# Optimization experiments

Measured on AMD Instinct MI355X. Metric: run time of the kernel, lower is better.

## Reference

```python
import jax, jax.numpy as jnp
import numpy as np

E_MAX = 8192  # fixed pad for the data-dependent edge count (jit-safe)
N_HITS = 8192


def setup_inputs() -> dict:
    key = jax.random.key(0)
    k1, k2, k3, k4, k5 = jax.random.split(key, 5)
    # columns: [event, x, y, z, station, track]
    r = jax.random.uniform(k1, (N_HITS,), minval=270.0, maxval=580.0)
    phi = jax.random.uniform(k2, (N_HITS,), minval=-3.1, maxval=3.1)
    # original uses phi = atan2(x, y), so x = r*sin(phi), y = r*cos(phi)
    x = r * jnp.sin(phi)
    y = r * jnp.cos(phi)
    z = jax.random.uniform(k3, (N_HITS,), minval=-2000.0, maxval=2000.0)
    station = jax.random.randint(k4, (N_HITS,), 0, 32).astype(jnp.float32)
    track = jax.random.randint(k5, (N_HITS,), 0, 1024).astype(jnp.float32)
    ev = jnp.zeros((N_HITS,), jnp.float32)  # single event -> one output graph
    event_data = jnp.stack([ev, x, y, z, station, track], axis=1)
    return {"event_data": event_data}


def _convert_normalize(event_data):
    # convert(): cartesian -> (r, phi, z); note atan2(x, y) as in the source
    x, y, z = event_data[:, 1], event_data[:, 2], event_data[:, 3]
    r = jnp.sqrt(x * x + y * y)
    phi = jnp.arctan2(x, y)
    # normalize() with hard-coded constraints [[269,581],[-3.15,3.15],[-2386,2386]]
    rn = 2.0 * (r - 269.0) / (581.0 - 269.0) - 1.0
    phin = 2.0 * (phi + 3.15) / (2.0 * 3.15) - 1.0
    zn = 2.0 * (z + 2386.0) / (2.0 * 2386.0) - 1.0
    return rn, phin, zn


def reference(event_data):
    rn, phin, zn = _convert_normalize(event_data)
    ev = event_data[:, 0].astype(jnp.int32)
    st = event_data[:, 4].astype(jnp.int32)
    # pair (i, j) valid iff same event and station_j == station_i + 1
    pair = (ev[:, None] == ev[None, :]) & (st[:, None] == (st[None, :] - 1))
    # merged[:, -2] = phi_j - phi_i ; merged[:, -1] = z_j - z_i (normalized coords)
    dphi = phin[None, :] - phin[:, None]  # [N, N]
    dz = zn[None, :] - zn[:, None]        # [N, N]
    valid = pair & (dphi > -0.04) & (dphi < 0.04) & (dz > -0.03) & (dz < 0.03)
    # torch.nonzero equivalent, padded to E_MAX (row-major order matches torch)
    src, dst = jnp.nonzero(valid, size=E_MAX, fill_value=0)
    count = jnp.sum(valid)
    edge_mask = jnp.arange(E_MAX) < count  # True for real edges, False for pads

    track = event_data[:, 5]
    # edges[:, [index_prev, index_current]] = track ids of (prev hit, next hit)
    edges = jnp.stack([track[src], track[dst]], axis=1)  # [E_MAX, 2]
    X = jnp.stack([rn, phin, zn], axis=1)  # hits[:, [1,2,3]] / 1.0
    # Ri/Ro: incidence via broadcast equality of track ids, as in the source
    Ri = ((track[:, None] == edges[None, :, 1]) & edge_mask[None, :]).astype(jnp.int32)
    Ro = ((track[:, None] == edges[None, :, 0]) & edge_mask[None, :]).astype(jnp.int32)
    y_lbl = jnp.zeros((E_MAX,), jnp.float32)
    return X, Ri, Ro, y_lbl, edges, edge_mask
```

## Files before the change

kernel.cpp:

```cpp
#include <hip/hip_runtime.h>

#define N_HITS 8192
#define E_MAX  8192
#define NSTA   32
#define NTRK   1024
#define NCHUNK 128

#define WS_HITA    0
#define WS_HTRACK  131072
#define WS_CAND    163840
#define WS_CCNT    294912
#define WS_COFF    311296
#define WS_BSTART  327680
#define WS_RCNT    327936
#define WS_ROFF    360704
#define WS_TCNT    393472
#define WS_TFILL   397568
#define WS_TOFF    401664
#define WS_THITS   405760

#define OFF_X  0
#define OFF_RI 24576
#define OFF_RO 67133440
#define OFF_Y  134242304
#define OFF_E  134250496
#define OFF_M  134266880

__global__ void k_pre(const float* __restrict__ ed, float* __restrict__ out,
                      float4* __restrict__ hitA, float* __restrict__ htrack,
                      int* __restrict__ ccnt, int* __restrict__ tcnt) {
    int h = blockIdx.x * blockDim.x + threadIdx.x;
    int lane = threadIdx.x & 63;
    int w = h >> 6;
    const float* row = ed + h * 6;
    float ev = row[0], x = row[1], y = row[2], z = row[3], stf = row[4], tr = row[5];
    float r   = sqrtf(x * x + y * y);
    float phi = atan2f(x, y);
    float rn   = 2.0f * (r   - 269.0f)  / 312.0f  - 1.0f;
    float phin = 2.0f * (phi + 3.15f)   / 6.3f    - 1.0f;
    float zn   = 2.0f * (z   + 2386.0f) / 4772.0f - 1.0f;
    out[OFF_X + h * 3 + 0] = rn;
    out[OFF_X + h * 3 + 1] = phin;
    out[OFF_X + h * 3 + 2] = zn;
    int st = (int)stf;
    hitA[h] = make_float4(phin, zn, (float)(int)ev, stf);
    htrack[h] = tr;
    for (int b = 0; b < NSTA; ++b) {
        unsigned long long m = __ballot(st == b);
        if (lane == 0) ccnt[b * NCHUNK + w] = __popcll(m);
    }
    atomicAdd(&tcnt[(int)tr], 1);
}

__global__ void k_scans(const int* __restrict__ ccnt, int* __restrict__ coff,
                        int* __restrict__ bstart,
                        const int* __restrict__ tcnt, int* __restrict__ toff) {
    __shared__ int sums[256];
    int tid = threadIdx.x;
    {
        int base = tid * 16;
        int loc[16]; int s = 0;
        for (int k = 0; k < 16; ++k) { loc[k] = ccnt[base + k]; s += loc[k]; }
        sums[tid] = s; __syncthreads();
        for (int d = 1; d < 256; d <<= 1) {
            int v = (tid >= d) ? sums[tid - d] : 0;
            __syncthreads();
            sums[tid] += v;
            __syncthreads();
        }
        int run = sums[tid] - s;
        for (int k = 0; k < 16; ++k) { coff[base + k] = run; run += loc[k]; }
        __syncthreads();
        if (tid < NSTA) bstart[tid] = coff[tid * NCHUNK];
        if (tid == 0)   bstart[NSTA] = N_HITS;
        __syncthreads();
    }
    {
        int base = tid * 4;
        int loc[4]; int s = 0;
        for (int k = 0; k < 4; ++k) { loc[k] = tcnt[base + k]; s += loc[k]; }
        sums[tid] = s; __syncthreads();
        for (int d = 1; d < 256; d <<= 1) {
            int v = (tid >= d) ? sums[tid - d] : 0;
            __syncthreads();
            sums[tid] += v;
            __syncthreads();
        }
        int run = sums[tid] - s;
        for (int k = 0; k < 4; ++k) { toff[base + k] = run; run += loc[k]; }
    }
}

__global__ void k_scatter(const float4* __restrict__ hitA, const float* __restrict__ htrack,
                          const int* __restrict__ coff, float4* __restrict__ cand,
                          const int* __restrict__ toff, int* __restrict__ tfill,
                          int* __restrict__ thits) {
    int h = blockIdx.x * blockDim.x + threadIdx.x;
    int lane = threadIdx.x & 63;
    int w = h >> 6;
    float4 a = hitA[h];
    float tr = htrack[h];
    int st = (int)a.w;
    for (int b = 0; b < NSTA; ++b) {
        unsigned long long m = __ballot(st == b);
        if (st == b) {
            int rank = __popcll(m & ((1ull << lane) - 1ull));
            cand[coff[b * NCHUNK + w] + rank] = make_float4(a.x, a.y, a.z, tr);
        }
    }
    int ti = (int)tr;
    int pos = atomicAdd(&tfill[ti], 1);
    thits[toff[ti] + pos] = h;
}

__device__ __forceinline__ bool edge_pred(float4 me, float4 cj) {
    float dphi = cj.x - me.x;
    float dz   = cj.y - me.y;
    return (cj.z == me.z) & (dphi > -0.04f) & (dphi < 0.04f)
                          & (dz > -0.03f) & (dz < 0.03f);
}

__global__ void k_rowcount(const float4* __restrict__ hitA, const float4* __restrict__ cand,
                           const int* __restrict__ bstart, int* __restrict__ rcnt) {
    int tid = threadIdx.x;
    int lane = tid & 63;
    int row = blockIdx.x * (blockDim.x >> 6) + (tid >> 6);
    float4 me = hitA[row];
    int b = (int)me.w + 1;
    int cnt = 0;
    if (b >= 1 && b < NSTA) {
        int s = bstart[b], e = bstart[b + 1];
        for (int k0 = s; k0 < e; k0 += 64) {
            int kk = k0 + lane;
            bool p = false;
            if (kk < e) p = edge_pred(me, cand[kk]);
            cnt += __popcll(__ballot(p));
        }
    }
    if (lane == 0) rcnt[row] = cnt;
}

__global__ void k_scanrows(const int* __restrict__ rcnt, int* __restrict__ roff,
                           const float* __restrict__ htrack, float* __restrict__ out) {
    __shared__ int sums[256];
    int tid = threadIdx.x;
    int base = tid * 32;
    int loc[32]; int s = 0;
    for (int k = 0; k < 32; ++k) { loc[k] = rcnt[base + k]; s += loc[k]; }
    sums[tid] = s; __syncthreads();
    for (int d = 1; d < 256; d <<= 1) {
        int v = (tid >= d) ? sums[tid - d] : 0;
        __syncthreads();
        sums[tid] += v;
        __syncthreads();
    }
    int run = sums[tid] - s;
    for (int k = 0; k < 32; ++k) { roff[base + k] = run; run += loc[k]; }
    __syncthreads();
    int S = sums[255];
    float t0 = htrack[0];
    for (int e = tid; e < E_MAX; e += 256) {
        bool v = e < S;
        out[OFF_M + e] = v ? 1.0f : 0.0f;
        if (!v) {
            out[OFF_E + 2 * e]     = t0;
            out[OFF_E + 2 * e + 1] = t0;
        }
    }
}

__global__ void k_emit(const float4* __restrict__ hitA, const float* __restrict__ htrack,
                       const float4* __restrict__ cand, const int* __restrict__ bstart,
                       const int* __restrict__ roff, const int* __restrict__ toff,
                       const int* __restrict__ tcnt, const int* __restrict__ thits,
                       float* __restrict__ out) {
    int tid = threadIdx.x;
    int lane = tid & 63;
    int row = blockIdx.x * (blockDim.x >> 6) + (tid >> 6);
    float4 me = hitA[row];
    int b = (int)me.w + 1;
    if (b < 1 || b >= NSTA) return;
    float tr_i = htrack[row];
    int bo = (int)tr_i;
    int os = toff[bo], oc = tcnt[bo];
    int s = bstart[b], e = bstart[b + 1];
    int base = roff[row];
    int c = 0;
    for (int k0 = s; k0 < e; k0 += 64) {
        int kk = k0 + lane;
        float4 cj = make_float4(0.f, 0.f, 0.f, 0.f);
        bool p = false;
        if (kk < e) { cj = cand[kk]; p = edge_pred(me, cj); }
        unsigned long long m = __ballot(p);
        if (p) {
            int idx = base + c + __popcll(m & ((1ull << lane) - 1ull));
            if (idx < E_MAX) {
                out[OFF_E + 2 * idx]     = tr_i;
                out[OFF_E + 2 * idx + 1] = cj.w;
                for (int j = 0; j < oc; ++j)
                    out[OFF_RO + (size_t)thits[os + j] * E_MAX + idx] = 1.0f;
                int bi = (int)cj.w;
                int is = toff[bi], ic = tcnt[bi];
                for (int j = 0; j < ic; ++j)
                    out[OFF_RI + (size_t)thits[is + j] * E_MAX + idx] = 1.0f;
            }
        }
        c += __popcll(m);
    }
}

extern "C" void kernel_launch(void* const* d_in, const int* in_sizes, int n_in,
                              void* d_out, int out_size, void* d_ws, size_t ws_size,
                              hipStream_t stream) {
    const float* ed = (const float*)d_in[0];
    float* out = (float*)d_out;
    char* ws = (char*)d_ws;

    float4* hitA   = (float4*)(ws + WS_HITA);
    float*  htrack = (float*) (ws + WS_HTRACK);
    float4* cand   = (float4*)(ws + WS_CAND);
    int*    ccnt   = (int*)   (ws + WS_CCNT);
    int*    coff   = (int*)   (ws + WS_COFF);
    int*    bstart = (int*)   (ws + WS_BSTART);
    int*    rcnt   = (int*)   (ws + WS_RCNT);
    int*    roffp  = (int*)   (ws + WS_ROFF);
    int*    tcnt   = (int*)   (ws + WS_TCNT);
    int*    tfill  = (int*)   (ws + WS_TFILL);
    int*    toff   = (int*)   (ws + WS_TOFF);
    int*    thits  = (int*)   (ws + WS_THITS);

    hipMemsetAsync(out + OFF_RI, 0, (size_t)(OFF_E - OFF_RI) * sizeof(float), stream);
    hipMemsetAsync(ws + WS_TCNT, 0, 2 * NTRK * sizeof(int), stream);

    hipLaunchKernelGGL(k_pre,      dim3(32),   dim3(256), 0, stream, ed, out, hitA, htrack, ccnt, tcnt);
    hipLaunchKernelGGL(k_scans,    dim3(1),    dim3(256), 0, stream, ccnt, coff, bstart, tcnt, toff);
    hipLaunchKernelGGL(k_scatter,  dim3(32),   dim3(256), 0, stream, hitA, htrack, coff, cand, toff, tfill, thits);
    hipLaunchKernelGGL(k_rowcount, dim3(2048), dim3(256), 0, stream, hitA, cand, bstart, rcnt);
    hipLaunchKernelGGL(k_scanrows, dim3(1),    dim3(256), 0, stream, rcnt, roffp, htrack, out);
    hipLaunchKernelGGL(k_emit,     dim3(2048), dim3(256), 0, stream, hitA, htrack, cand, bstart, roffp, toff, tcnt, thits, out);
}
```

Before: 556.4 us.

## Fuse six pipeline kernels into one cooperative kernel with grid syncs

Replaces the six separate launches (preprocess, scans, scatter, row count, row scan, emit) with a single cooperative kernel that separates phases using grid-wide syncs. The goal is to remove per-launch overhead and the gaps between dependent small kernels. In exchange, the grid shrinks to 256 blocks, so each wave handles 8 rows in the count and emit phases. This reduces parallelism for the latency-bound scattered writes, and single-block scan phases leave most of the grid idle at each barrier.

```diff
diff --git a/kernel.cpp b/kernel.cpp
--- a/kernel.cpp
+++ b/kernel.cpp
@@ -1,4 +1,6 @@
 #include <hip/hip_runtime.h>
+#include <hip/hip_cooperative_groups.h>
+namespace cg = cooperative_groups;
 
 #define N_HITS 8192
 #define E_MAX  8192
@@ -26,93 +28,6 @@
 #define OFF_E  134250496
 #define OFF_M  134266880
 
-__global__ void k_pre(const float* __restrict__ ed, float* __restrict__ out,
-                      float4* __restrict__ hitA, float* __restrict__ htrack,
-                      int* __restrict__ ccnt, int* __restrict__ tcnt) {
-    int h = blockIdx.x * blockDim.x + threadIdx.x;
-    int lane = threadIdx.x & 63;
-    int w = h >> 6;
-    const float* row = ed + h * 6;
-    float ev = row[0], x = row[1], y = row[2], z = row[3], stf = row[4], tr = row[5];
-    float r   = sqrtf(x * x + y * y);
-    float phi = atan2f(x, y);
-    float rn   = 2.0f * (r   - 269.0f)  / 312.0f  - 1.0f;
-    float phin = 2.0f * (phi + 3.15f)   / 6.3f    - 1.0f;
-    float zn   = 2.0f * (z   + 2386.0f) / 4772.0f - 1.0f;
-    out[OFF_X + h * 3 + 0] = rn;
-    out[OFF_X + h * 3 + 1] = phin;
-    out[OFF_X + h * 3 + 2] = zn;
-    int st = (int)stf;
-    hitA[h] = make_float4(phin, zn, (float)(int)ev, stf);
-    htrack[h] = tr;
-    for (int b = 0; b < NSTA; ++b) {
-        unsigned long long m = __ballot(st == b);
-        if (lane == 0) ccnt[b * NCHUNK + w] = __popcll(m);
-    }
-    atomicAdd(&tcnt[(int)tr], 1);
-}
-
-__global__ void k_scans(const int* __restrict__ ccnt, int* __restrict__ coff,
-                        int* __restrict__ bstart,
-                        const int* __restrict__ tcnt, int* __restrict__ toff) {
-    __shared__ int sums[256];
-    int tid = threadIdx.x;
-    {
-        int base = tid * 16;
-        int loc[16]; int s = 0;
-        for (int k = 0; k < 16; ++k) { loc[k] = ccnt[base + k]; s += loc[k]; }
-        sums[tid] = s; __syncthreads();
-        for (int d = 1; d < 256; d <<= 1) {
-            int v = (tid >= d) ? sums[tid - d] : 0;
-            __syncthreads();
-            sums[tid] += v;
-            __syncthreads();
-        }
-        int run = sums[tid] - s;
-        for (int k = 0; k < 16; ++k) { coff[base + k] = run; run += loc[k]; }
-        __syncthreads();
-        if (tid < NSTA) bstart[tid] = coff[tid * NCHUNK];
-        if (tid == 0)   bstart[NSTA] = N_HITS;
-        __syncthreads();
-    }
-    {
-        int base = tid * 4;
-        int loc[4]; int s = 0;
-        for (int k = 0; k < 4; ++k) { loc[k] = tcnt[base + k]; s += loc[k]; }
-        sums[tid] = s; __syncthreads();
-        for (int d = 1; d < 256; d <<= 1) {
-            int v = (tid >= d) ? sums[tid - d] : 0;
-            __syncthreads();
-            sums[tid] += v;
-            __syncthreads();
-        }
-        int run = sums[tid] - s;
-        for (int k = 0; k < 4; ++k) { toff[base + k] = run; run += loc[k]; }
-    }
-}
-
-__global__ void k_scatter(const float4* __restrict__ hitA, const float* __restrict__ htrack,
-                          const int* __restrict__ coff, float4* __restrict__ cand,
-                          const int* __restrict__ toff, int* __restrict__ tfill,
-                          int* __restrict__ thits) {
-    int h = blockIdx.x * blockDim.x + threadIdx.x;
-    int lane = threadIdx.x & 63;
-    int w = h >> 6;
-    float4 a = hitA[h];
-    float tr = htrack[h];
-    int st = (int)a.w;
-    for (int b = 0; b < NSTA; ++b) {
-        unsigned long long m = __ballot(st == b);
-        if (st == b) {
-            int rank = __popcll(m & ((1ull << lane) - 1ull));
-            cand[coff[b * NCHUNK + w] + rank] = make_float4(a.x, a.y, a.z, tr);
-        }
-    }
-    int ti = (int)tr;
-    int pos = atomicAdd(&tfill[ti], 1);
-    thits[toff[ti] + pos] = h;
-}
-
 __device__ __forceinline__ bool edge_pred(float4 me, float4 cj) {
     float dphi = cj.x - me.x;
     float dz   = cj.y - me.y;
@@ -120,102 +35,8 @@
                           & (dz > -0.03f) & (dz < 0.03f);
 }
 
-__global__ void k_rowcount(const float4* __restrict__ hitA, const float4* __restrict__ cand,
-                           const int* __restrict__ bstart, int* __restrict__ rcnt) {
-    int tid = threadIdx.x;
-    int lane = tid & 63;
-    int row = blockIdx.x * (blockDim.x >> 6) + (tid >> 6);
-    float4 me = hitA[row];
-    int b = (int)me.w + 1;
-    int cnt = 0;
-    if (b >= 1 && b < NSTA) {
-        int s = bstart[b], e = bstart[b + 1];
-        for (int k0 = s; k0 < e; k0 += 64) {
-            int kk = k0 + lane;
-            bool p = false;
-            if (kk < e) p = edge_pred(me, cand[kk]);
-            cnt += __popcll(__ballot(p));
-        }
-    }
-    if (lane == 0) rcnt[row] = cnt;
-}
-
-__global__ void k_scanrows(const int* __restrict__ rcnt, int* __restrict__ roff,
-                           const float* __restrict__ htrack, float* __restrict__ out) {
-    __shared__ int sums[256];
-    int tid = threadIdx.x;
-    int base = tid * 32;
-    int loc[32]; int s = 0;
-    for (int k = 0; k < 32; ++k) { loc[k] = rcnt[base + k]; s += loc[k]; }
-    sums[tid] = s; __syncthreads();
-    for (int d = 1; d < 256; d <<= 1) {
-        int v = (tid >= d) ? sums[tid - d] : 0;
-        __syncthreads();
-        sums[tid] += v;
-        __syncthreads();
-    }
-    int run = sums[tid] - s;
-    for (int k = 0; k < 32; ++k) { roff[base + k] = run; run += loc[k]; }
-    __syncthreads();
-    int S = sums[255];
-    float t0 = htrack[0];
-    for (int e = tid; e < E_MAX; e += 256) {
-        bool v = e < S;
-        out[OFF_M + e] = v ? 1.0f : 0.0f;
-        if (!v) {
-            out[OFF_E + 2 * e]     = t0;
-            out[OFF_E + 2 * e + 1] = t0;
-        }
-    }
-}
-
-__global__ void k_emit(const float4* __restrict__ hitA, const float* __restrict__ htrack,
-                       const float4* __restrict__ cand, const int* __restrict__ bstart,
-                       const int* __restrict__ roff, const int* __restrict__ toff,
-                       const int* __restrict__ tcnt, const int* __restrict__ thits,
-                       float* __restrict__ out) {
-    int tid = threadIdx.x;
-    int lane = tid & 63;
-    int row = blockIdx.x * (blockDim.x >> 6) + (tid >> 6);
-    float4 me = hitA[row];
-    int b = (int)me.w + 1;
-    if (b < 1 || b >= NSTA) return;
-    float tr_i = htrack[row];
-    int bo = (int)tr_i;
-    int os = toff[bo], oc = tcnt[bo];
-    int s = bstart[b], e = bstart[b + 1];
-    int base = roff[row];
-    int c = 0;
-    for (int k0 = s; k0 < e; k0 += 64) {
-        int kk = k0 + lane;
-        float4 cj = make_float4(0.f, 0.f, 0.f, 0.f);
-        bool p = false;
-        if (kk < e) { cj = cand[kk]; p = edge_pred(me, cj); }
-        unsigned long long m = __ballot(p);
-        if (p) {
-            int idx = base + c + __popcll(m & ((1ull << lane) - 1ull));
-            if (idx < E_MAX) {
-                out[OFF_E + 2 * idx]     = tr_i;
-                out[OFF_E + 2 * idx + 1] = cj.w;
-                for (int j = 0; j < oc; ++j)
-                    out[OFF_RO + (size_t)thits[os + j] * E_MAX + idx] = 1.0f;
-                int bi = (int)cj.w;
-                int is = toff[bi], ic = tcnt[bi];
-                for (int j = 0; j < ic; ++j)
-                    out[OFF_RI + (size_t)thits[is + j] * E_MAX + idx] = 1.0f;
-            }
-        }
-        c += __popcll(m);
-    }
-}
-
-extern "C" void kernel_launch(void* const* d_in, const int* in_sizes, int n_in,
-                              void* d_out, int out_size, void* d_ws, size_t ws_size,
-                              hipStream_t stream) {
-    const float* ed = (const float*)d_in[0];
-    float* out = (float*)d_out;
-    char* ws = (char*)d_ws;
-
+__global__ void k_all(const float* __restrict__ ed, float* __restrict__ out,
+                      char* __restrict__ ws) {
     float4* hitA   = (float4*)(ws + WS_HITA);
     float*  htrack = (float*) (ws + WS_HTRACK);
     float4* cand   = (float4*)(ws + WS_CAND);
@@ -223,19 +44,180 @@
     int*    coff   = (int*)   (ws + WS_COFF);
     int*    bstart = (int*)   (ws + WS_BSTART);
     int*    rcnt   = (int*)   (ws + WS_RCNT);
-    int*    roffp  = (int*)   (ws + WS_ROFF);
+    int*    roff   = (int*)   (ws + WS_ROFF);
     int*    tcnt   = (int*)   (ws + WS_TCNT);
     int*    tfill  = (int*)   (ws + WS_TFILL);
     int*    toff   = (int*)   (ws + WS_TOFF);
     int*    thits  = (int*)   (ws + WS_THITS);
 
+    cg::grid_group grid = cg::this_grid();
+    __shared__ int sums[256];
+    int tid  = threadIdx.x;
+    int t    = blockIdx.x * 256 + tid;
+    int lane = tid & 63;
+    int gw   = t >> 6;
+
+    if (t < N_HITS) {
+        int h = t, w = h >> 6;
+        const float* row = ed + h * 6;
+        float ev = row[0], x = row[1], y = row[2], z = row[3], stf = row[4], tr = row[5];
+        float r   = sqrtf(x * x + y * y);
+        float phi = atan2f(x, y);
+        float rn   = 2.0f * (r   - 269.0f)  / 312.0f  - 1.0f;
+        float phin = 2.0f * (phi + 3.15f)   / 6.3f    - 1.0f;
+        float zn   = 2.0f * (z   + 2386.0f) / 4772.0f - 1.0f;
+        out[OFF_X + h * 3 + 0] = rn;
+        out[OFF_X + h * 3 + 1] = phin;
+        out[OFF_X + h * 3 + 2] = zn;
+        int st = (int)stf;
+        hitA[h] = make_float4(phin, zn, (float)(int)ev, stf);
+        htrack[h] = tr;
+        for (int b = 0; b < NSTA; ++b) {
+            unsigned long long m = __ballot(st == b);
+            if (lane == 0) ccnt[b * NCHUNK + w] = __popcll(m);
+        }
+        atomicAdd(&tcnt[(int)tr], 1);
+    }
+    grid.sync();
+
+    if (blockIdx.x == 0) {
+        {
+            int base = tid * 16;
+            int loc[16]; int s = 0;
+            for (int k = 0; k < 16; ++k) { loc[k] = ccnt[base + k]; s += loc[k]; }
+            sums[tid] = s; __syncthreads();
+            for (int d = 1; d < 256; d <<= 1) {
+                int v = (tid >= d) ? sums[tid - d] : 0;
+                __syncthreads(); sums[tid] += v; __syncthreads();
+            }
+            int run = sums[tid] - s;
+            for (int k = 0; k < 16; ++k) { coff[base + k] = run; run += loc[k]; }
+            __syncthreads();
+            if (tid < NSTA) bstart[tid] = coff[tid * NCHUNK];
+            if (tid == 0)   bstart[NSTA] = N_HITS;
+            __syncthreads();
+        }
+        {
+            int base = tid * 4;
+            int loc[4]; int s = 0;
+            for (int k = 0; k < 4; ++k) { loc[k] = tcnt[base + k]; s += loc[k]; }
+            sums[tid] = s; __syncthreads();
+            for (int d = 1; d < 256; d <<= 1) {
+                int v = (tid >= d) ? sums[tid - d] : 0;
+                __syncthreads(); sums[tid] += v; __syncthreads();
+            }
+            int run = sums[tid] - s;
+            for (int k = 0; k < 4; ++k) { toff[base + k] = run; run += loc[k]; }
+        }
+    }
+    grid.sync();
+
+    if (t < N_HITS) {
+        int h = t, w = h >> 6;
+        float4 a = hitA[h];
+        float tr = htrack[h];
+        int st = (int)a.w;
+        for (int b = 0; b < NSTA; ++b) {
+            unsigned long long m = __ballot(st == b);
+            if (st == b) {
+                int rank = __popcll(m & ((1ull << lane) - 1ull));
+                cand[coff[b * NCHUNK + w] + rank] = make_float4(a.x, a.y, a.z, tr);
+            }
+        }
+        int ti = (int)tr;
+        int pos = atomicAdd(&tfill[ti], 1);
+        thits[toff[ti] + pos] = h;
+    }
+    grid.sync();
+
+    for (int r = 0; r < 8; ++r) {
+        int row = gw * 8 + r;
+        float4 me = hitA[row];
+        int b = (int)me.w + 1;
+        int cnt = 0;
+        if (b >= 1 && b < NSTA) {
+            int s = bstart[b], e = bstart[b + 1];
+            for (int k0 = s; k0 < e; k0 += 64) {
+                int kk = k0 + lane;
+                bool p = false;
+                if (kk < e) p = edge_pred(me, cand[kk]);
+                cnt += __popcll(__ballot(p));
+            }
+        }
+        if (lane == 0) rcnt[row] = cnt;
+    }
+    grid.sync();
+
+    if (blockIdx.x == 0) {
+        int base = tid * 32;
+        int loc[32]; int s = 0;
+        for (int k = 0; k < 32; ++k) { loc[k] = rcnt[base + k]; s += loc[k]; }
+        sums[tid] = s; __syncthreads();
+        for (int d = 1; d < 256; d <<= 1) {
+            int v = (tid >= d) ? sums[tid - d] : 0;
+            __syncthreads(); sums[tid] += v; __syncthreads();
+        }
+        int run = sums[tid] - s;
+        for (int k = 0; k < 32; ++k) { roff[base + k] = run; run += loc[k]; }
+        __syncthreads();
+        int S = sums[255];
+        float t0 = htrack[0];
+        for (int e = tid; e < E_MAX; e += 256) {
+            bool v = e < S;
+            out[OFF_M + e] = v ? 1.0f : 0.0f;
+            if (!v) {
+                out[OFF_E + 2 * e]     = t0;
+                out[OFF_E + 2 * e + 1] = t0;
+            }
+        }
+    }
+    grid.sync();
+
+    for (int r = 0; r < 8; ++r) {
+        int row = gw * 8 + r;
+        float4 me = hitA[row];
+        int b = (int)me.w + 1;
+        if (b < 1 || b >= NSTA) continue;
+        float tr_i = htrack[row];
+        int bo = (int)tr_i;
+        int os = toff[bo], oc = tcnt[bo];
+        int s = bstart[b], e = bstart[b + 1];
+        int base = roff[row];
+        int c = 0;
+        for (int k0 = s; k0 < e; k0 += 64) {
+            int kk = k0 + lane;
+            float4 cj = make_float4(0.f, 0.f, 0.f, 0.f);
+            bool p = false;
+            if (kk < e) { cj = cand[kk]; p = edge_pred(me, cj); }
+            unsigned long long m = __ballot(p);
+            if (p) {
+                int idx = base + c + __popcll(m & ((1ull << lane) - 1ull));
+                if (idx < E_MAX) {
+                    out[OFF_E + 2 * idx]     = tr_i;
+                    out[OFF_E + 2 * idx + 1] = cj.w;
+                    for (int j = 0; j < oc; ++j)
+                        out[OFF_RO + (size_t)thits[os + j] * E_MAX + idx] = 1.0f;
+                    int bi = (int)cj.w;
+                    int is = toff[bi], ic = tcnt[bi];
+                    for (int j = 0; j < ic; ++j)
+                        out[OFF_RI + (size_t)thits[is + j] * E_MAX + idx] = 1.0f;
+                }
+            }
+            c += __popcll(m);
+        }
+    }
+}
+
+extern "C" void kernel_launch(void* const* d_in, const int* in_sizes, int n_in,
+                              void* d_out, int out_size, void* d_ws, size_t ws_size,
+                              hipStream_t stream) {
+    const float* ed = (const float*)d_in[0];
+    float* out = (float*)d_out;
+    char* ws = (char*)d_ws;
+
     hipMemsetAsync(out + OFF_RI, 0, (size_t)(OFF_E - OFF_RI) * sizeof(float), stream);
     hipMemsetAsync(ws + WS_TCNT, 0, 2 * NTRK * sizeof(int), stream);
 
-    hipLaunchKernelGGL(k_pre,      dim3(32),   dim3(256), 0, stream, ed, out, hitA, htrack, ccnt, tcnt);
-    hipLaunchKernelGGL(k_scans,    dim3(1),    dim3(256), 0, stream, ccnt, coff, bstart, tcnt, toff);
-    hipLaunchKernelGGL(k_scatter,  dim3(32),   dim3(256), 0, stream, hitA, htrack, coff, cand, toff, tfill, thits);
-    hipLaunchKernelGGL(k_rowcount, dim3(2048), dim3(256), 0, stream, hitA, cand, bstart, rcnt);
-    hipLaunchKernelGGL(k_scanrows, dim3(1),    dim3(256), 0, stream, rcnt, roffp, htrack, out);
-    hipLaunchKernelGGL(k_emit,     dim3(2048), dim3(256), 0, stream, hitA, htrack, cand, bstart, roffp, toff, tcnt, thits, out);
+    void* args[] = {(void*)&ed, (void*)&out, (void*)&ws};
+    hipLaunchCooperativeKernel((void*)k_all, dim3(256), dim3(256), args, 0, stream);
 }
```

Measured after the change: 705.1 us. 26.7% more time.

## Fuse zero-fill into preprocessing kernel and merge scans with scatter

Applied to the files above, without the earlier changes.

Replaces the two hipMemsetAsync calls with a custom nontemporal vectorized zero-fill performed by extra blocks of the preprocessing kernel. The per-track histogram moves from global atomics into shared memory inside a single-block kernel, which also absorbs the scatter step, cutting two launches. The cost is that the scatter now runs serially on one block instead of 32, and the ~537 MB fill is bandwidth-bound either way, so any gain comes mainly from overlap and fewer launches.

```diff
diff --git a/kernel.cpp b/kernel.cpp
--- a/kernel.cpp
+++ b/kernel.cpp
@@ -5,6 +5,8 @@
 #define NSTA   32
 #define NTRK   1024
 #define NCHUNK 128
+
+typedef float v4f __attribute__((ext_vector_type(4)));
 
 #define WS_HITA    0
 #define WS_HTRACK  131072
@@ -15,9 +17,8 @@
 #define WS_RCNT    327936
 #define WS_ROFF    360704
 #define WS_TCNT    393472
-#define WS_TFILL   397568
-#define WS_TOFF    401664
-#define WS_THITS   405760
+#define WS_TOFF    397568
+#define WS_THITS   401664
 
 #define OFF_X  0
 #define OFF_RI 24576
@@ -26,49 +27,73 @@
 #define OFF_E  134250496
 #define OFF_M  134266880
 
-__global__ void k_pre(const float* __restrict__ ed, float* __restrict__ out,
-                      float4* __restrict__ hitA, float* __restrict__ htrack,
-                      int* __restrict__ ccnt, int* __restrict__ tcnt) {
-    int h = blockIdx.x * blockDim.x + threadIdx.x;
-    int lane = threadIdx.x & 63;
-    int w = h >> 6;
-    const float* row = ed + h * 6;
-    float ev = row[0], x = row[1], y = row[2], z = row[3], stf = row[4], tr = row[5];
-    float r   = sqrtf(x * x + y * y);
-    float phi = atan2f(x, y);
-    float rn   = 2.0f * (r   - 269.0f)  / 312.0f  - 1.0f;
-    float phin = 2.0f * (phi + 3.15f)   / 6.3f    - 1.0f;
-    float zn   = 2.0f * (z   + 2386.0f) / 4772.0f - 1.0f;
-    out[OFF_X + h * 3 + 0] = rn;
-    out[OFF_X + h * 3 + 1] = phin;
-    out[OFF_X + h * 3 + 2] = zn;
-    int st = (int)stf;
-    hitA[h] = make_float4(phin, zn, (float)(int)ev, stf);
-    htrack[h] = tr;
-    for (int b = 0; b < NSTA; ++b) {
-        unsigned long long m = __ballot(st == b);
-        if (lane == 0) ccnt[b * NCHUNK + w] = __popcll(m);
-    }
-    atomicAdd(&tcnt[(int)tr], 1);
-}
-
-__global__ void k_scans(const int* __restrict__ ccnt, int* __restrict__ coff,
-                        int* __restrict__ bstart,
-                        const int* __restrict__ tcnt, int* __restrict__ toff) {
-    __shared__ int sums[256];
-    int tid = threadIdx.x;
+#define NFILL4 33556480
+
+__global__ void __launch_bounds__(256) k_pre_fill(const float* __restrict__ ed,
+                                                  float* __restrict__ out,
+                                                  float4* __restrict__ hitA,
+                                                  float* __restrict__ htrack,
+                                                  int* __restrict__ ccnt) {
+    int bid = blockIdx.x;
+    int tid = threadIdx.x;
+    if (bid < 32) {
+        int h = bid * 256 + tid;
+        int lane = tid & 63;
+        int w = h >> 6;
+        const float* row = ed + h * 6;
+        float ev = row[0], x = row[1], y = row[2], z = row[3], stf = row[4], tr = row[5];
+        float r   = sqrtf(x * x + y * y);
+        float phi = atan2f(x, y);
+        float rn   = 2.0f * (r   - 269.0f)  / 312.0f  - 1.0f;
+        float phin = 2.0f * (phi + 3.15f)   / 6.3f    - 1.0f;
+        float zn   = 2.0f * (z   + 2386.0f) / 4772.0f - 1.0f;
+        out[OFF_X + h * 3 + 0] = rn;
+        out[OFF_X + h * 3 + 1] = phin;
+        out[OFF_X + h * 3 + 2] = zn;
+        int st = (int)stf;
+        hitA[h] = make_float4(phin, zn, (float)(int)ev, stf);
+        htrack[h] = tr;
+        for (int b = 0; b < NSTA; ++b) {
+            unsigned long long m = __ballot(st == b);
+            if (lane == 0) ccnt[b * NCHUNK + w] = __popcll(m);
+        }
+    } else {
+        v4f z4 = {0.f, 0.f, 0.f, 0.f};
+        v4f* dst = (v4f*)(out + OFF_RI);
+        size_t i = (size_t)(bid - 32) * 256 + tid;
+        const size_t stride = (size_t)2048 * 256;
+        for (; i < NFILL4; i += stride)
+            __builtin_nontemporal_store(z4, dst + i);
+    }
+}
+
+__global__ void __launch_bounds__(256) k_scan_scatter(const float4* __restrict__ hitA,
+                                                      const float* __restrict__ htrack,
+                                                      const int* __restrict__ ccnt,
+                                                      int* __restrict__ coff,
+                                                      int* __restrict__ bstart,
+                                                      float4* __restrict__ cand,
+                                                      int* __restrict__ tcnt,
+                                                      int* __restrict__ toff,
+                                                      int* __restrict__ thits) {
+    __shared__ int s_sums[256];
+    __shared__ int s_tc[NTRK];
+    __shared__ int s_to[NTRK];
+    __shared__ int s_tf[NTRK];
+    int tid = threadIdx.x;
+    int lane = tid & 63;
+    int wv = tid >> 6;
+
     {
         int base = tid * 16;
         int loc[16]; int s = 0;
         for (int k = 0; k < 16; ++k) { loc[k] = ccnt[base + k]; s += loc[k]; }
-        sums[tid] = s; __syncthreads();
+        s_sums[tid] = s; __syncthreads();
         for (int d = 1; d < 256; d <<= 1) {
-            int v = (tid >= d) ? sums[tid - d] : 0;
-            __syncthreads();
-            sums[tid] += v;
-            __syncthreads();
-        }
-        int run = sums[tid] - s;
+            int v = (tid >= d) ? s_sums[tid - d] : 0;
+            __syncthreads(); s_sums[tid] += v; __syncthreads();
+        }
+        int run = s_sums[tid] - s;
         for (int k = 0; k < 16; ++k) { coff[base + k] = run; run += loc[k]; }
         __syncthreads();
         if (tid < NSTA) bstart[tid] = coff[tid * NCHUNK];
@@ -76,41 +101,45 @@
         __syncthreads();
     }
     {
+        for (int k = tid; k < NTRK; k += 256) s_tc[k] = 0;
+        __syncthreads();
+        for (int k = 0; k < 32; ++k)
+            atomicAdd(&s_tc[(int)htrack[tid + 256 * k]], 1);
+        __syncthreads();
         int base = tid * 4;
         int loc[4]; int s = 0;
-        for (int k = 0; k < 4; ++k) { loc[k] = tcnt[base + k]; s += loc[k]; }
-        sums[tid] = s; __syncthreads();
+        for (int k = 0; k < 4; ++k) { loc[k] = s_tc[base + k]; s += loc[k]; }
+        s_sums[tid] = s; __syncthreads();
         for (int d = 1; d < 256; d <<= 1) {
-            int v = (tid >= d) ? sums[tid - d] : 0;
-            __syncthreads();
-            sums[tid] += v;
-            __syncthreads();
-        }
-        int run = sums[tid] - s;
-        for (int k = 0; k < 4; ++k) { toff[base + k] = run; run += loc[k]; }
-    }
-}
-
-__global__ void k_scatter(const float4* __restrict__ hitA, const float* __restrict__ htrack,
-                          const int* __restrict__ coff, float4* __restrict__ cand,
-                          const int* __restrict__ toff, int* __restrict__ tfill,
-                          int* __restrict__ thits) {
-    int h = blockIdx.x * blockDim.x + threadIdx.x;
-    int lane = threadIdx.x & 63;
-    int w = h >> 6;
-    float4 a = hitA[h];
-    float tr = htrack[h];
-    int st = (int)a.w;
-    for (int b = 0; b < NSTA; ++b) {
-        unsigned long long m = __ballot(st == b);
-        if (st == b) {
-            int rank = __popcll(m & ((1ull << lane) - 1ull));
-            cand[coff[b * NCHUNK + w] + rank] = make_float4(a.x, a.y, a.z, tr);
-        }
-    }
-    int ti = (int)tr;
-    int pos = atomicAdd(&tfill[ti], 1);
-    thits[toff[ti] + pos] = h;
+            int v = (tid >= d) ? s_sums[tid - d] : 0;
+            __syncthreads(); s_sums[tid] += v; __syncthreads();
+        }
+        int run = s_sums[tid] - s;
+        for (int k = 0; k < 4; ++k) {
+            s_to[base + k] = run;
+            toff[base + k] = run;
+            tcnt[base + k] = loc[k];
+            s_tf[base + k] = 0;
+            run += loc[k];
+        }
+        __syncthreads();
+    }
+    for (int c = wv; c < NCHUNK; c += 4) {
+        int h = c * 64 + lane;
+        float4 a = hitA[h];
+        float tr = htrack[h];
+        int st = (int)a.w;
+        for (int b = 0; b < NSTA; ++b) {
+            unsigned long long m = __ballot(st == b);
+            if (st == b) {
+                int rank = __popcll(m & ((1ull << lane) - 1ull));
+                cand[coff[b * NCHUNK + c] + rank] = make_float4(a.x, a.y, a.z, tr);
+            }
+        }
+        int ti = (int)tr;
+        int pos = atomicAdd(&s_tf[ti], 1);
+        thits[s_to[ti] + pos] = h;
+    }
 }
 
 __device__ __forceinline__ bool edge_pred(float4 me, float4 cj) {
@@ -120,11 +149,13 @@
                           & (dz > -0.03f) & (dz < 0.03f);
 }
 
-__global__ void k_rowcount(const float4* __restrict__ hitA, const float4* __restrict__ cand,
-                           const int* __restrict__ bstart, int* __restrict__ rcnt) {
+__global__ void __launch_bounds__(256) k_rowcount(const float4* __restrict__ hitA,
+                                                  const float4* __restrict__ cand,
+                                                  const int* __restrict__ bstart,
+                                                  int* __restrict__ rcnt) {
     int tid = threadIdx.x;
     int lane = tid & 63;
-    int row = blockIdx.x * (blockDim.x >> 6) + (tid >> 6);
+    int row = blockIdx.x * 4 + (tid >> 6);
     float4 me = hitA[row];
     int b = (int)me.w + 1;
     int cnt = 0;
@@ -140,8 +171,10 @@
     if (lane == 0) rcnt[row] = cnt;
 }
 
-__global__ void k_scanrows(const int* __restrict__ rcnt, int* __restrict__ roff,
-                           const float* __restrict__ htrack, float* __restrict__ out) {
+__global__ void __launch_bounds__(256) k_scanrows(const int* __restrict__ rcnt,
+                                                  int* __restrict__ roff,
+                                                  const float* __restrict__ htrack,
+                                                  float* __restrict__ out) {
     __shared__ int sums[256];
     int tid = threadIdx.x;
     int base = tid * 32;
@@ -150,9 +183,7 @@
     sums[tid] = s; __syncthreads();
     for (int d = 1; d < 256; d <<= 1) {
         int v = (tid >= d) ? sums[tid - d] : 0;
-        __syncthreads();
-        sums[tid] += v;
-        __syncthreads();
+        __syncthreads(); sums[tid] += v; __syncthreads();
     }
     int run = sums[tid] - s;
     for (int k = 0; k < 32; ++k) { roff[base + k] = run; run += loc[k]; }
@@ -169,14 +200,18 @@
     }
 }
 
-__global__ void k_emit(const float4* __restrict__ hitA, const float* __restrict__ htrack,
-                       const float4* __restrict__ cand, const int* __restrict__ bstart,
-                       const int* __restrict__ roff, const int* __restrict__ toff,
-                       const int* __restrict__ tcnt, const int* __restrict__ thits,
-                       float* __restrict__ out) {
+__global__ void __launch_bounds__(256) k_emit(const float4* __restrict__ hitA,
+                                              const float* __restrict__ htrack,
+                                              const float4* __restrict__ cand,
+                                              const int* __restrict__ bstart,
+                                              const int* __restrict__ roff,
+                                              const int* __restrict__ toff,
+                                              const int* __restrict__ tcnt,
+                                              const int* __restrict__ thits,
+                                              float* __restrict__ out) {
     int tid = threadIdx.x;
     int lane = tid & 63;
-    int row = blockIdx.x * (blockDim.x >> 6) + (tid >> 6);
+    int row = blockIdx.x * 4 + (tid >> 6);
     float4 me = hitA[row];
     int b = (int)me.w + 1;
     if (b < 1 || b >= NSTA) return;
@@ -225,17 +260,12 @@
     int*    rcnt   = (int*)   (ws + WS_RCNT);
     int*    roffp  = (int*)   (ws + WS_ROFF);
     int*    tcnt   = (int*)   (ws + WS_TCNT);
-    int*    tfill  = (int*)   (ws + WS_TFILL);
     int*    toff   = (int*)   (ws + WS_TOFF);
     int*    thits  = (int*)   (ws + WS_THITS);
 
-    hipMemsetAsync(out + OFF_RI, 0, (size_t)(OFF_E - OFF_RI) * sizeof(float), stream);
-    hipMemsetAsync(ws + WS_TCNT, 0, 2 * NTRK * sizeof(int), stream);
-
-    hipLaunchKernelGGL(k_pre,      dim3(32),   dim3(256), 0, stream, ed, out, hitA, htrack, ccnt, tcnt);
-    hipLaunchKernelGGL(k_scans,    dim3(1),    dim3(256), 0, stream, ccnt, coff, bstart, tcnt, toff);
-    hipLaunchKernelGGL(k_scatter,  dim3(32),   dim3(256), 0, stream, hitA, htrack, coff, cand, toff, tfill, thits);
-    hipLaunchKernelGGL(k_rowcount, dim3(2048), dim3(256), 0, stream, hitA, cand, bstart, rcnt);
-    hipLaunchKernelGGL(k_scanrows, dim3(1),    dim3(256), 0, stream, rcnt, roffp, htrack, out);
-    hipLaunchKernelGGL(k_emit,     dim3(2048), dim3(256), 0, stream, hitA, htrack, cand, bstart, roffp, toff, tcnt, thits, out);
-}
+    hipLaunchKernelGGL(k_pre_fill,    dim3(2080), dim3(256), 0, stream, ed, out, hitA, htrack, ccnt);
+    hipLaunchKernelGGL(k_scan_scatter,dim3(1),    dim3(256), 0, stream, hitA, htrack, ccnt, coff, bstart, cand, tcnt, toff, thits);
+    hipLaunchKernelGGL(k_rowcount,    dim3(2048), dim3(256), 0, stream, hitA, cand, bstart, rcnt);
+    hipLaunchKernelGGL(k_scanrows,    dim3(1),    dim3(256), 0, stream, rcnt, roffp, htrack, out);
+    hipLaunchKernelGGL(k_emit,        dim3(2048), dim3(256), 0, stream, hitA, htrack, cand, bstart, roffp, toff, tcnt, thits, out);
+}
```

After: 748.7 us. 1.35x slower.
